# Performance work log

Measured on AMD Instinct MI355X. Metric: run time of the kernel, lower is better.

The kernel has to match this reference:

```python
import jax, jax.numpy as jnp
import numpy as np

B = 32        # graphs per batch
MAXN = 2048   # max nodes per graph (dense batch length)
HEADS = 8
DH = 64       # head dim (512/8)
M = 256       # FAVOR+ random features
D = 512
EPS = 1e-5    # batchnorm eps
KEPS = 1e-6   # performer stabilizer


def _batchnorm(x, g, b):
    # torch BatchNorm1d training-mode: biased batch statistics over node dim
    mu = jnp.mean(x, axis=0)
    var = jnp.mean((x - mu) ** 2, axis=0)
    return (x - mu) * jax.lax.rsqrt(var + EPS) * g + b


def setup_inputs() -> dict:
    key = jax.random.key(0)
    ks = jax.random.split(key, 10)
    sizes = 1024 + (np.arange(B) * 131) % 1025   # ragged graph sizes in [1024, 2048]
    N = int(sizes.sum())                          # 48544
    E = N * 8
    batch = jnp.asarray(np.repeat(np.arange(B), sizes), dtype=jnp.int32)
    edge_index = jax.random.randint(ks[0], (2, E), 0, N, dtype=jnp.int32)
    s = 1.0 / np.sqrt(D)
    return {
        'x': jax.random.normal(ks[1], (N, D), jnp.float32),
        'batch': batch,
        'edge_index': edge_index,
        'norm1_g': jnp.ones((D,), jnp.float32),
        'norm1_b': jnp.zeros((D,), jnp.float32),
        'norm2_g': jnp.ones((D,), jnp.float32),
        'norm2_b': jnp.zeros((D,), jnp.float32),
        'W_conv': jax.random.normal(ks[2], (D, D), jnp.float32) * s,
        'b_conv': jnp.zeros((D,), jnp.float32),
        'Wq': jax.random.normal(ks[3], (D, D), jnp.float32) * s,
        'Wk': jax.random.normal(ks[4], (D, D), jnp.float32) * s,
        'Wv': jax.random.normal(ks[5], (D, D), jnp.float32) * s,
        'Wo': jax.random.normal(ks[6], (D, D), jnp.float32) * s,
        'proj': jax.random.normal(ks[7], (M, DH), jnp.float32),
    }


def _forward(x, batch, edge_index, norm1_g, norm1_b, norm2_g, norm2_b,
             W_conv, b_conv, Wq, Wk, Wv, Wo, proj):
    N = x.shape[0]
    E = edge_index.shape[1]
    h = x

    # norm1 (+ dropout p=0 -> identity) then local GNN conv (mean-agg GCN + linear + relu)
    xn = _batchnorm(x, norm1_g, norm1_b)
    msg = xn[edge_index[0]]                                        # [E, D] gather
    agg = jax.ops.segment_sum(msg, edge_index[1], num_segments=N)  # [N, D] scatter-add
    deg = jax.ops.segment_sum(jnp.ones((E,), x.dtype), edge_index[1], num_segments=N)
    agg = agg / jnp.maximum(deg, 1.0)[:, None]
    conv_out = jax.nn.relu(agg @ W_conv + b_conv)

    # to_dense_batch(h, batch) -> h_dense [B, MAXN, D], mask [B, MAXN]
    counts = jax.ops.segment_sum(jnp.ones((N,), jnp.int32), batch, num_segments=B)
    offsets = jnp.concatenate([jnp.zeros((1,), jnp.int32), jnp.cumsum(counts)[:-1]])
    pos = jnp.arange(N, dtype=jnp.int32) - offsets[batch]
    h_dense = jnp.zeros((B, MAXN, D), x.dtype).at[batch, pos].set(h)
    mask = jnp.zeros((B, MAXN), bool).at[batch, pos].set(True)

    # Performer FAVOR+ non-causal self-attention
    def heads(t, W):
        return (t @ W).reshape(B, MAXN, HEADS, DH).transpose(0, 2, 1, 3)  # [B,H,MAXN,DH]
    q, k, v = heads(h_dense, Wq), heads(h_dense, Wk), heads(h_dense, Wv)

    scale = DH ** -0.25  # data normalizer applied to q and k each

    def phi(t, is_query):
        t = t * scale
        u = jnp.einsum('bhnd,md->bhnm', t, proj)           # [B,H,MAXN,M]
        diag = 0.5 * jnp.sum(t * t, axis=-1, keepdims=True)
        if is_query:
            m_ = jnp.max(u, axis=-1, keepdims=True)
        else:
            m_ = jnp.max(u, axis=(-2, -1), keepdims=True)
        return jnp.exp(u - diag - jax.lax.stop_gradient(m_)) / np.sqrt(M) + KEPS

    qf = phi(q, True)
    kf = phi(k, False) * mask[:, None, :, None]   # zero padded keys
    vm = v * mask[:, None, :, None]

    kv = jnp.einsum('bhnm,bhnd->bhmd', kf, vm)                    # [B,H,M,DH]
    z = 1.0 / (jnp.einsum('bhnm,bhm->bhn', qf, kf.sum(axis=2)) + KEPS)
    attn = jnp.einsum('bhnm,bhmd->bhnd', qf, kv) * z[..., None]   # [B,H,MAXN,DH]
    attn = attn.transpose(0, 2, 1, 3).reshape(B, MAXN, D) @ Wo

    h_attn = attn[batch, pos]                                      # gather back: [mask]

    return _batchnorm(conv_out + h_attn + h, norm2_g, norm2_b)


def reference(x, batch, edge_index, norm1_g, norm1_b, norm2_g, norm2_b,
              W_conv, b_conv, Wq, Wk, Wv, Wo, proj):
    return _forward(x, batch, edge_index, norm1_g, norm1_b, norm2_g, norm2_b,
                    W_conv, b_conv, Wq, Wk, Wv, Wo, proj)
```

## Files before the change

kernel.cpp:

```cpp
#include <hip/hip_runtime.h>
#include <stdint.h>

#define CDIV(a,b) (((a)+(b)-1)/(b))

typedef __attribute__((ext_vector_type(4))) float f32x4;
typedef __attribute__((ext_vector_type(8))) short s16x8;
typedef __attribute__((ext_vector_type(8))) unsigned short u16x8;
typedef __attribute__((ext_vector_type(4))) unsigned short u16x4;

__device__ __forceinline__ float bf2f(unsigned short u) {
  union { unsigned int i; float f; } c; c.i = ((unsigned int)u) << 16; return c.f;
}
__device__ __forceinline__ unsigned short f2bf(float f) {
  union { float f; unsigned int i; } c; c.f = f;
  unsigned int u = c.i;
  u += 0x7fffu + ((u >> 16) & 1u);
  return (unsigned short)(u >> 16);
}

#define KVROWS 80

template<int BM, int BN, int WM, int WN, int EPI, int GSWAP>
__global__ __launch_bounds__(256) void gemm_bt(
    const unsigned short* __restrict__ A, const unsigned short* __restrict__ B,
    void* __restrict__ Cout, const float* __restrict__ aux,
    int K, int lda, int ldb, int ldc, long zsC, int Mstore)
{
  constexpr int MT = BM / (WM * 16);
  constexpr int NT = BN / (WN * 16);
  constexpr int LDT = 40;
  __shared__ unsigned short As[BM * LDT];
  __shared__ unsigned short Bs[BN * LDT];
  const int tid = threadIdx.x, wid = tid >> 6, lane = tid & 63;
  const int l15 = lane & 15, hi = lane >> 4;
  const int wr = wid / WN, wc = wid % WN;
  const int bx = GSWAP ? blockIdx.y : blockIdx.x;
  const int by = GSWAP ? blockIdx.x : blockIdx.y;
  long m0 = (long)by * BM;
  const int n0 = bx * BN;
  f32x4 acc[MT][NT] = {};
  for (int k0 = 0; k0 < K; k0 += 32) {
    #pragma unroll
    for (int c = tid; c < BM * 4; c += 256) {
      int row = c >> 2, c8 = (c & 3) * 8;
      *(u16x8*)(&As[row * LDT + c8]) = *(const u16x8*)(A + (m0 + row) * lda + k0 + c8);
    }
    #pragma unroll
    for (int c = tid; c < BN * 4; c += 256) {
      int row = c >> 2, c8 = (c & 3) * 8;
      *(u16x8*)(&Bs[row * LDT + c8]) = *(const u16x8*)(B + (long)(n0 + row) * ldb + k0 + c8);
    }
    __syncthreads();
    s16x8 af[MT], bfv[NT];
    #pragma unroll
    for (int mt = 0; mt < MT; mt++)
      af[mt] = *(const s16x8*)(&As[(wr * MT * 16 + mt * 16 + l15) * LDT + hi * 8]);
    #pragma unroll
    for (int nt = 0; nt < NT; nt++)
      bfv[nt] = *(const s16x8*)(&Bs[(wc * NT * 16 + nt * 16 + l15) * LDT + hi * 8]);
    #pragma unroll
    for (int mt = 0; mt < MT; mt++)
      #pragma unroll
      for (int nt = 0; nt < NT; nt++)
        acc[mt][nt] = __builtin_amdgcn_mfma_f32_16x16x32_bf16(bfv[nt], af[mt], acc[mt][nt], 0, 0, 0);
    __syncthreads();
  }
  #pragma unroll
  for (int mt = 0; mt < MT; mt++) {
    long r = m0 + wr * (MT * 16) + mt * 16 + l15;
    if (r < Mstore) {
      #pragma unroll
      for (int nt = 0; nt < NT; nt++) {
        const int col0 = n0 + wc * (NT * 16) + nt * 16 + hi * 4;
        f32x4 v = acc[mt][nt];
        if constexpr (EPI == 7) {
          u16x4 o;
          #pragma unroll
          for (int i = 0; i < 4; i++) o[i] = f2bf(v[i]);
          *(u16x4*)((unsigned short*)Cout + (long)(col0 >> 6) * zsC + r * 64 + (col0 & 63)) = o;
        } else if constexpr (EPI == 8) {
          const f32x4 ax = *(const f32x4*)(aux + r * ldc + col0);
          f32x4 o;
          #pragma unroll
          for (int i = 0; i < 4; i++) o[i] = v[i] + ax[i];
          *(f32x4*)((float*)Cout + r * ldc + col0) = o;
        }
      }
    }
  }
}

__global__ __launch_bounds__(256) void gemm_conv_bn(
    const unsigned short* __restrict__ A, const unsigned short* __restrict__ B,
    float* __restrict__ out, const float* __restrict__ bias,
    float* __restrict__ s1, float* __restrict__ s2, int Mstore)
{
  constexpr int LDT = 40;
  __shared__ unsigned short As[128 * LDT];
  __shared__ unsigned short Bs[128 * LDT];
  const int tid = threadIdx.x, wid = tid >> 6, lane = tid & 63;
  const int l15 = lane & 15, hi = lane >> 4;
  const int wr = wid >> 1, wc = wid & 1;
  long m0 = (long)blockIdx.y * 128;
  const int n0 = blockIdx.x * 128;
  f32x4 acc[4][4] = {};
  for (int k0 = 0; k0 < 512; k0 += 32) {
    #pragma unroll
    for (int c = tid; c < 512; c += 256) {
      int row = c >> 2, c8 = (c & 3) * 8;
      *(u16x8*)(&As[row * LDT + c8]) = *(const u16x8*)(A + (m0 + row) * 512 + k0 + c8);
      *(u16x8*)(&Bs[row * LDT + c8]) = *(const u16x8*)(B + (long)(n0 + row) * 512 + k0 + c8);
    }
    __syncthreads();
    s16x8 af[4], bfv[4];
    #pragma unroll
    for (int mt = 0; mt < 4; mt++)
      af[mt] = *(const s16x8*)(&As[(wr * 64 + mt * 16 + l15) * LDT + hi * 8]);
    #pragma unroll
    for (int nt = 0; nt < 4; nt++)
      bfv[nt] = *(const s16x8*)(&Bs[(wc * 64 + nt * 16 + l15) * LDT + hi * 8]);
    #pragma unroll
    for (int mt = 0; mt < 4; mt++)
      #pragma unroll
      for (int nt = 0; nt < 4; nt++)
        acc[mt][nt] = __builtin_amdgcn_mfma_f32_16x16x32_bf16(bfv[nt], af[mt], acc[mt][nt], 0, 0, 0);
    __syncthreads();
  }
  float st[4][4] = {};
  float sq[4][4] = {};
  #pragma unroll
  for (int mt = 0; mt < 4; mt++) {
    long r = m0 + wr * 64 + mt * 16 + l15;
    bool valid = r < Mstore;
    #pragma unroll
    for (int nt = 0; nt < 4; nt++) {
      const int col0 = n0 + wc * 64 + nt * 16 + hi * 4;
      f32x4 o = {0.f, 0.f, 0.f, 0.f};
      if (valid) {
        float* cp = out + r * 512 + col0;
        f32x4 cur = *(f32x4*)cp;
        #pragma unroll
        for (int i = 0; i < 4; i++) {
          float cv = acc[mt][nt][i] + bias[col0 + i];
          cv = cv > 0.f ? cv : 0.f;
          o[i] = cur[i] + cv;
        }
        *(f32x4*)cp = o;
      }
      #pragma unroll
      for (int i = 0; i < 4; i++) { st[nt][i] += o[i]; sq[nt][i] += o[i] * o[i]; }
    }
  }
  #pragma unroll
  for (int nt = 0; nt < 4; nt++)
    #pragma unroll
    for (int i = 0; i < 4; i++) {
      float a = st[nt][i], b = sq[nt][i];
      a += __shfl_xor(a, 1); a += __shfl_xor(a, 2); a += __shfl_xor(a, 4); a += __shfl_xor(a, 8);
      b += __shfl_xor(b, 1); b += __shfl_xor(b, 2); b += __shfl_xor(b, 4); b += __shfl_xor(b, 8);
      if (l15 == 0) {
        const int col = n0 + wc * 64 + nt * 16 + hi * 4 + i;
        atomicAdd(&s1[col], a);
        atomicAdd(&s2[col], b);
      }
    }
}

__global__ __launch_bounds__(256, 4) void k_kmax(
    const unsigned short* __restrict__ kvqh, const unsigned short* __restrict__ projb,
    const unsigned int* __restrict__ offs, unsigned int* __restrict__ kmax, long Npad) {
  __shared__ float wmax[4];
  const int tid = threadIdx.x, wid = tid >> 6, lane = tid & 63;
  const int bh = blockIdx.x & 255, xb = blockIdx.x >> 8;
  const int b = bh >> 3, h = bh & 7;
  const unsigned int off = offs[b];
  const int nb = (int)(offs[b + 1] - off);
  const int m0 = xb * 64;
  if (m0 >= nb) return;
  const unsigned short* A = kvqh + ((long)(8 + h) * Npad + off + m0) * 64;
  f32x4 acc[4][4] = {};
  #pragma unroll
  for (int k0 = 0; k0 < 64; k0 += 32) {
    s16x8 af[4], bfv[4];
    #pragma unroll
    for (int mt = 0; mt < 4; mt++)
      af[mt] = *(const s16x8*)(A + (long)(mt * 16 + (lane & 15)) * 64 + k0 + ((lane >> 4) * 8));
    #pragma unroll
    for (int nt = 0; nt < 4; nt++)
      bfv[nt] = *(const s16x8*)(projb + (long)(wid * 64 + nt * 16 + (lane & 15)) * 64 + k0 + ((lane >> 4) * 8));
    #pragma unroll
    for (int mt = 0; mt < 4; mt++)
      #pragma unroll
      for (int nt = 0; nt < 4; nt++)
        acc[mt][nt] = __builtin_amdgcn_mfma_f32_16x16x32_bf16(af[mt], bfv[nt], acc[mt][nt], 0, 0, 0);
  }
  float bm = -3.0e38f;
  #pragma unroll
  for (int mt = 0; mt < 4; mt++)
    #pragma unroll
    for (int i = 0; i < 4; i++) {
      int row = mt * 16 + ((lane >> 4) << 2) + i;
      if (m0 + row < nb) {
        #pragma unroll
        for (int nt = 0; nt < 4; nt++) bm = fmaxf(bm, acc[mt][nt][i]);
      }
    }
  #pragma unroll
  for (int s = 1; s < 64; s <<= 1) bm = fmaxf(bm, __shfl_xor(bm, s));
  if (lane == 0) wmax[wid] = bm;
  __syncthreads();
  if (tid == 0) {
    float m = fmaxf(fmaxf(wmax[0], wmax[1]), fmaxf(wmax[2], wmax[3]));
    atomicMax(&kmax[b * 8 + h], __float_as_uint(fmaxf(m, 0.f)));
  }
}

__global__ __launch_bounds__(256) void k_kvm(
    const unsigned short* __restrict__ kvqh, const unsigned short* __restrict__ projb,
    const unsigned int* __restrict__ offs, const unsigned int* __restrict__ kmax,
    unsigned short* __restrict__ kvTb, long Npad) {
  constexpr int TLD = 72;
  __shared__ unsigned short vsT[2][64 * TLD];
  __shared__ unsigned short kfsT[64 * TLD];
  const int tid = threadIdx.x, wid = tid >> 6, lane = tid & 63;
  const int bh = blockIdx.x & 255, mblk = blockIdx.x >> 8;
  const int b = bh >> 3, h = bh & 7;
  const unsigned int off = offs[b];
  const int nb = (int)(offs[b + 1] - off);
  const float km = __uint_as_float(kmax[b * 8 + h]);
  const unsigned short* Kp = kvqh + ((long)(8 + h) * Npad + off) * 64;
  const unsigned short* Vp = kvqh + ((long)(16 + h) * Npad + off) * 64;
  const unsigned short* Pp = projb + (long)(mblk * 64 + wid * 16) * 64;
  const int l15 = lane & 15, hi = lane >> 4;
  const int mloc = wid * 16 + l15;

  #pragma unroll
  for (int c = tid; c < 512; c += 256) {
    int row = c >> 3, c8 = (c & 7) * 8;
    int rot = (c & 7) * 8;
    u16x8 v = *(const u16x8*)(Vp + (long)row * 64 + c8);
    #pragma unroll
    for (int j = 0; j < 8; j++) vsT[0][(c8 + j) * TLD + ((row + rot) & 63)] = v[j];
  }
  __syncthreads();

  f32x4 akv[4] = {};
  float ksum = 0.f;
  int buf = 0;
  for (int n0 = 0; n0 < nb; n0 += 64) {
    f32x4 acc[4] = {};
    float dsum[4] = {0.f, 0.f, 0.f, 0.f};
    #pragma unroll
    for (int k0 = 0; k0 < 64; k0 += 32) {
      s16x8 af[4];
      #pragma unroll
      for (int mt = 0; mt < 4; mt++)
        af[mt] = *(const s16x8*)(Kp + ((long)n0 + mt * 16 + l15) * 64 + k0 + hi * 8);
      s16x8 bfv = *(const s16x8*)(Pp + (long)l15 * 64 + k0 + hi * 8);
      #pragma unroll
      for (int mt = 0; mt < 4; mt++) {
        #pragma unroll
        for (int j = 0; j < 8; j++) {
          float a = bf2f((unsigned short)af[mt][j]);
          dsum[mt] += a * a;
        }
        acc[mt] = __builtin_amdgcn_mfma_f32_16x16x32_bf16(af[mt], bfv, acc[mt], 0, 0, 0);
      }
    }
    float rs[4];
    #pragma unroll
    for (int mt = 0; mt < 4; mt++) {
      float s = dsum[mt];
      s += __shfl_xor(s, 16); s += __shfl_xor(s, 32);
      rs[mt] = 0.0625f * s;
    }
    #pragma unroll
    for (int mt = 0; mt < 4; mt++) {
      int r0 = mt * 16 + hi * 4;
      float e[4];
      #pragma unroll
      for (int i = 0; i < 4; i++) {
        float dg = __shfl(rs[mt], hi * 4 + i);
        e[i] = (n0 + r0 + i < nb) ? (__expf(acc[mt][i] - dg - km) * 0.0625f + 1e-6f) : 0.f;
      }
      ksum += e[0] + e[1] + e[2] + e[3];
      unsigned int p0 = (unsigned int)f2bf(e[0]) | ((unsigned int)f2bf(e[1]) << 16);
      unsigned int p1 = (unsigned int)f2bf(e[2]) | ((unsigned int)f2bf(e[3]) << 16);
      *(unsigned int*)(&kfsT[mloc * TLD + r0]) = p0;
      *(unsigned int*)(&kfsT[mloc * TLD + r0 + 2]) = p1;
    }
    if (n0 + 64 < nb) {
      #pragma unroll
      for (int c = tid; c < 512; c += 256) {
        int row = c >> 3, c8 = (c & 7) * 8;
        int rot = (c & 7) * 8;
        u16x8 v = *(const u16x8*)(Vp + ((long)n0 + 64 + row) * 64 + c8);
        #pragma unroll
        for (int j = 0; j < 8; j++) vsT[buf ^ 1][(c8 + j) * TLD + ((row + rot) & 63)] = v[j];
      }
    }
    #pragma unroll
    for (int ks = 0; ks < 2; ks++) {
      s16x8 bB = *(const s16x8*)(&kfsT[mloc * TLD + ks * 32 + hi * 8]);
      #pragma unroll
      for (int mt2 = 0; mt2 < 4; mt2++) {
        int d = mt2 * 16 + l15;
        int rrot = ((ks * 32 + hi * 8) + ((d >> 3) & 7) * 8) & 63;
        s16x8 aA = *(const s16x8*)(&vsT[buf][d * TLD + rrot]);
        akv[mt2] = __builtin_amdgcn_mfma_f32_16x16x32_bf16(aA, bB, akv[mt2], 0, 0, 0);
      }
    }
    __syncthreads();
    buf ^= 1;
  }
  long base = ((long)b * 8 + h) * (KVROWS * 256);
  const int m = mblk * 64 + mloc;
  #pragma unroll
  for (int mt2 = 0; mt2 < 4; mt2++)
    #pragma unroll
    for (int i = 0; i < 4; i++) {
      int d = mt2 * 16 + hi * 4 + i;
      kvTb[base + (long)d * 256 + m] = f2bf(akv[mt2][i]);
    }
  ksum += __shfl_xor(ksum, 16); ksum += __shfl_xor(ksum, 32);
  if (hi == 0) kvTb[base + 64 * 256 + m] = f2bf(ksum);
}

__global__ __launch_bounds__(256, 4) void k_qflash(
    const unsigned short* __restrict__ qh_all, const unsigned short* __restrict__ projb,
    const unsigned short* __restrict__ kvTb, const unsigned int* __restrict__ offs,
    unsigned short* __restrict__ attn, long Npad) {
  constexpr int QLDT = 264;
  __shared__ unsigned short qfs[64 * QLDT];
  __shared__ float sdiag[64];
  __shared__ float smax[4][64];
  const int tid = threadIdx.x, wid = tid >> 6, lane = tid & 63;
  const int l15 = lane & 15, hi = lane >> 4;
  const int bh = blockIdx.x & 255, xb = blockIdx.x >> 8;
  const int b = bh >> 3, h = bh & 7;
  const unsigned int off = offs[b];
  const int nb = (int)(offs[b + 1] - off);
  const int m0 = xb * 64;
  if (m0 >= nb) return;
  const unsigned short* A = qh_all + ((long)h * Npad + off + m0) * 64;
  f32x4 acc[4][4] = {};
  float dsum[4] = {0.f, 0.f, 0.f, 0.f};
  #pragma unroll
  for (int k0 = 0; k0 < 64; k0 += 32) {
    s16x8 af[4], bfv[4];
    #pragma unroll
    for (int mt = 0; mt < 4; mt++)
      af[mt] = *(const s16x8*)(A + (long)(mt * 16 + l15) * 64 + k0 + hi * 8);
    #pragma unroll
    for (int nt = 0; nt < 4; nt++)
      bfv[nt] = *(const s16x8*)(projb + (long)(wid * 64 + nt * 16 + l15) * 64 + k0 + hi * 8);
    if (wid == 0) {
      #pragma unroll
      for (int mt = 0; mt < 4; mt++)
        #pragma unroll
        for (int j = 0; j < 8; j++) {
          float a = bf2f((unsigned short)af[mt][j]);
          dsum[mt] += a * a;
        }
    }
    #pragma unroll
    for (int mt = 0; mt < 4; mt++)
      #pragma unroll
      for (int nt = 0; nt < 4; nt++)
        acc[mt][nt] = __builtin_amdgcn_mfma_f32_16x16x32_bf16(af[mt], bfv[nt], acc[mt][nt], 0, 0, 0);
  }
  if (wid == 0) {
    #pragma unroll
    for (int mt = 0; mt < 4; mt++) {
      float s = dsum[mt];
      s += __shfl_xor(s, 16); s += __shfl_xor(s, 32);
      if (lane < 16) sdiag[mt * 16 + lane] = 0.0625f * s;
    }
  }
  #pragma unroll
  for (int mt = 0; mt < 4; mt++)
    #pragma unroll
    for (int i = 0; i < 4; i++) {
      float rm = fmaxf(fmaxf(acc[mt][0][i], acc[mt][1][i]), fmaxf(acc[mt][2][i], acc[mt][3][i]));
      rm = fmaxf(rm, __shfl_xor(rm, 1)); rm = fmaxf(rm, __shfl_xor(rm, 2));
      rm = fmaxf(rm, __shfl_xor(rm, 4)); rm = fmaxf(rm, __shfl_xor(rm, 8));
      if (l15 == 0) smax[wid][mt * 16 + hi * 4 + i] = rm;
    }
  __syncthreads();
  #pragma unroll
  for (int mt = 0; mt < 4; mt++)
    #pragma unroll
    for (int i = 0; i < 4; i++) {
      int row = mt * 16 + hi * 4 + i;
      float rm = fmaxf(fmaxf(smax[0][row], smax[1][row]), fmaxf(smax[2][row], smax[3][row]));
      float sub = sdiag[row] + rm;
      #pragma unroll
      for (int nt = 0; nt < 4; nt++) {
        int col = wid * 64 + nt * 16 + l15;
        qfs[row * QLDT + col] = f2bf(__expf(acc[mt][nt][i] - sub) * 0.0625f + 1e-6f);
      }
    }
  __syncthreads();
  const unsigned short* kvb = kvTb + ((long)b * 8 + h) * (KVROWS * 256);
  f32x4 acc2[4] = {};
  f32x4 acc3 = {};
  #pragma unroll
  for (int ks = 0; ks < 8; ks++) {
    s16x8 aq = *(const s16x8*)(&qfs[(wid * 16 + l15) * QLDT + ks * 32 + hi * 8]);
    #pragma unroll
    for (int t = 0; t < 4; t++) {
      s16x8 bk = *(const s16x8*)(kvb + (long)(t * 16 + l15) * 256 + ks * 32 + hi * 8);
      acc2[t] = __builtin_amdgcn_mfma_f32_16x16x32_bf16(aq, bk, acc2[t], 0, 0, 0);
    }
    s16x8 bz = *(const s16x8*)(kvb + (long)(64 + l15) * 256 + ks * 32 + hi * 8);
    acc3 = __builtin_amdgcn_mfma_f32_16x16x32_bf16(aq, bz, acc3, 0, 0, 0);
  }
  float zr[4];
  #pragma unroll
  for (int i = 0; i < 4; i++) {
    float zden = __shfl(acc3[i], hi * 16);
    zr[i] = 1.f / (zden + 1e-6f);
  }
  #pragma unroll
  for (int t = 0; t < 4; t++)
    #pragma unroll
    for (int i = 0; i < 4; i++) {
      int row = wid * 16 + hi * 4 + i;
      if (m0 + row < nb)
        attn[(long)(off + m0 + row) * 512 + h * 64 + t * 16 + l15] = f2bf(acc2[t][i] * zr[i]);
    }
}


__global__ void k_fill(float* __restrict__ out, long n, float v) {
  long i = (long)blockIdx.x * 256 + threadIdx.x;
  if (i < n) out[i] = v;
}

__global__ void k_convx_stats(const float* __restrict__ x, unsigned short* __restrict__ xb,
                              float* __restrict__ s1, float* __restrict__ s2, int N, int rpb) {
  int t = threadIdx.x;
  int r0 = blockIdx.x * rpb;
  int r1 = min(N, r0 + rpb);
  float a1 = 0, a2 = 0, b1 = 0, b2 = 0;
  for (int r = r0; r < r1; r++) {
    const float* xr = x + (long)r * 512 + 2 * t;
    float va = xr[0], vb = xr[1];
    a1 += va; a2 += va * va; b1 += vb; b2 += vb * vb;
    *(unsigned int*)(xb + (long)r * 512 + 2 * t) =
        (unsigned int)f2bf(va) | ((unsigned int)f2bf(vb) << 16);
  }
  atomicAdd(&s1[2 * t], a1); atomicAdd(&s2[2 * t], a2);
  atomicAdd(&s1[2 * t + 1], b1); atomicAdd(&s2[2 * t + 1], b2);
}

__global__ void k_transall(const float* __restrict__ w0, const float* __restrict__ w1,
                           const float* __restrict__ w2, const float* __restrict__ w3,
                           const float* __restrict__ w4, unsigned short* __restrict__ out) {
  long idx = (long)blockIdx.x * 256 + threadIdx.x;
  if (idx >= (5L << 18)) return;
  int which = (int)(idx >> 18);
  int r = (int)(idx & 262143);
  int n = r >> 9, k = r & 511;
  const float* w = which == 0 ? w0 : which == 1 ? w1 : which == 2 ? w2 : which == 3 ? w3 : w4;
  out[idx] = f2bf(w[k * 512 + n]);
}

__global__ void k_scale_copy_bf(const float* __restrict__ in, unsigned short* __restrict__ out,
                                int n, float scl) {
  int i = blockIdx.x * 256 + threadIdx.x;
  if (i < n) out[i] = f2bf(in[i] * scl);
}

__global__ void k_bn_final(const float* __restrict__ s1, const float* __restrict__ s2,
                           const float* __restrict__ g, const float* __restrict__ b,
                           float* __restrict__ a, float* __restrict__ c, float invN) {
  int t = threadIdx.x;
  float mu = s1[t] * invN;
  float var = s2[t] * invN - mu * mu;
  float inv = rsqrtf(var + 1e-5f);
  float av = g[t] * inv;
  a[t] = av;
  c[t] = b[t] - mu * av;
}

__global__ void k_deg(const int* __restrict__ ed, unsigned int* __restrict__ deg, long E) {
  long i = (long)blockIdx.x * 256 + threadIdx.x;
  if (i < E) atomicAdd(&deg[ed[i]], 1u);
}

__global__ void k_offs(const int* __restrict__ batch, unsigned int* __restrict__ offs, int N) {
  int i = blockIdx.x * 256 + threadIdx.x;
  if (i >= N) return;
  int b = batch[i];
  if (i == 0) { for (int bb = 0; bb <= b; bb++) offs[bb] = 0; }
  else {
    int pb = batch[i - 1];
    if (pb != b) for (int bb = pb + 1; bb <= b; bb++) offs[bb] = i;
  }
  if (i == N - 1) { for (int bb = b + 1; bb <= 32; bb++) offs[bb] = N; }
}

__global__ __launch_bounds__(1024) void k_scan_nodes(const unsigned int* __restrict__ deg,
                                                     unsigned int* __restrict__ rowstart, int N) {
  __shared__ unsigned int wsum[16];
  __shared__ unsigned int carry_s;
  int t = threadIdx.x, lane = t & 63, wid = t >> 6;
  if (t == 0) carry_s = 0;
  __syncthreads();
  for (int base = 0; base < N; base += 1024) {
    int i = base + t;
    unsigned int v = (i < N) ? deg[i] : 0;
    unsigned int sc = v;
    #pragma unroll
    for (int s = 1; s < 64; s <<= 1) {
      unsigned int u = __shfl_up(sc, s);
      if (lane >= s) sc += u;
    }
    if (lane == 63) wsum[wid] = sc;
    __syncthreads();
    unsigned int woff = 0, tot = 0;
    #pragma unroll
    for (int w = 0; w < 16; w++) { unsigned int s = wsum[w]; if (w < wid) woff += s; tot += s; }
    unsigned int carry = carry_s;
    if (i < N) rowstart[i] = carry + woff + sc - v;
    __syncthreads();
    if (t == 0) carry_s = carry + tot;
    __syncthreads();
  }
  if (threadIdx.x == 0) rowstart[N] = carry_s;
}

__global__ void k_csr_fill(const int* __restrict__ es, const int* __restrict__ ed,
                           const unsigned int* __restrict__ rowstart,
                           unsigned int* __restrict__ cursor, int* __restrict__ csr, long E) {
  long e = (long)blockIdx.x * 256 + threadIdx.x;
  if (e >= E) return;
  int d = ed[e];
  unsigned int slot = atomicAdd(&cursor[d], 1u);
  csr[rowstart[d] + slot] = es[e];
}

__global__ __launch_bounds__(128) void k_gather(const int* __restrict__ csr,
                                                const unsigned int* __restrict__ rowstart,
                                                const unsigned short* __restrict__ xb,
                                                const float* __restrict__ a1, const float* __restrict__ c1,
                                                unsigned short* __restrict__ conv_in, int N) {
  long n = blockIdx.x;
  int c = threadIdx.x * 4;
  u16x4 o; o[0] = 0; o[1] = 0; o[2] = 0; o[3] = 0;
  if (n < N) {
    unsigned int r0 = rowstart[n], r1 = rowstart[n + 1];
    if (r1 > r0) {
      f32x4 acc0 = {}, acc1 = {};
      unsigned int j = r0;
      for (; j + 2 <= r1; j += 2) {
        u16x4 v0 = *(const u16x4*)(xb + (long)csr[j] * 512 + c);
        u16x4 v1 = *(const u16x4*)(xb + (long)csr[j + 1] * 512 + c);
        #pragma unroll
        for (int i = 0; i < 4; i++) { acc0[i] += bf2f(v0[i]); acc1[i] += bf2f(v1[i]); }
      }
      if (j < r1) {
        u16x4 v0 = *(const u16x4*)(xb + (long)csr[j] * 512 + c);
        #pragma unroll
        for (int i = 0; i < 4; i++) acc0[i] += bf2f(v0[i]);
      }
      f32x4 acc = acc0 + acc1;
      float inv = 1.f / (float)(r1 - r0);
      o[0] = f2bf(acc[0] * inv * a1[c + 0] + c1[c + 0]);
      o[1] = f2bf(acc[1] * inv * a1[c + 1] + c1[c + 1]);
      o[2] = f2bf(acc[2] * inv * a1[c + 2] + c1[c + 2]);
      o[3] = f2bf(acc[3] * inv * a1[c + 3] + c1[c + 3]);
    }
  }
  *(u16x4*)(conv_in + n * 512 + c) = o;
}

__global__ void k_bn_apply(float* __restrict__ y, const float* __restrict__ a,
                           const float* __restrict__ c, long total) {
  long i4 = ((long)blockIdx.x * 256 + threadIdx.x) * 4;
  if (i4 >= total) return;
  int col = (int)(i4 & 511);
  f32x4 v = *(const f32x4*)(y + i4);
  #pragma unroll
  for (int j = 0; j < 4; j++) v[j] = v[j] * a[col + j] + c[col + j];
  *(f32x4*)(y + i4) = v;
}


extern "C" void kernel_launch(void* const* d_in, const int* in_sizes, int n_in,
                              void* d_out, int out_size, void* d_ws, size_t ws_size,
                              hipStream_t stream) {
  (void)n_in; (void)out_size;
  const float* x = (const float*)d_in[0];
  const int* batch = (const int*)d_in[1];
  const int* eidx = (const int*)d_in[2];
  const float* n1g = (const float*)d_in[3];
  const float* n1b = (const float*)d_in[4];
  const float* n2g = (const float*)d_in[5];
  const float* n2b = (const float*)d_in[6];
  const float* wconv = (const float*)d_in[7];
  const float* bconv = (const float*)d_in[8];
  const float* wq = (const float*)d_in[9];
  const float* wk = (const float*)d_in[10];
  const float* wv = (const float*)d_in[11];
  const float* wo = (const float*)d_in[12];
  const float* proj = (const float*)d_in[13];

  const int N = in_sizes[1];
  const long E = in_sizes[2] / 2;
  const long Npad = CDIV(N, 128) * 128 + 256;
  const int Mb = (int)((CDIV(N, 128) * 128 + 128) / 128);
  const int MbC = CDIV(N, 128);
  const int* es = eidx;
  const int* ed = eidx + E;
  float* out = (float*)d_out;

  char* p = (char*)d_ws;
  auto alloc = [&](size_t bytes) -> char* {
    char* r = p;
    p += (bytes + 255) & ~(size_t)255;
    return r;
  };
  unsigned short* kvqh = (unsigned short*)alloc((size_t)24 * Npad * 64 * 2);
  unsigned short* xbf  = (unsigned short*)alloc((size_t)Npad * 512 * 2);
  unsigned short* conv_in = (unsigned short*)alloc((size_t)Npad * 512 * 2);
  unsigned short* kvT_b = (unsigned short*)alloc((size_t)32 * 8 * KVROWS * 256 * 2);
  unsigned short* wts   = (unsigned short*)alloc((size_t)5 * 512 * 512 * 2);
  unsigned short* proj_s = (unsigned short*)alloc((size_t)256 * 64 * 2);
  float* bn1_acc = (float*)alloc(1024 * 4);
  float* bn1_ac  = (float*)alloc(1024 * 4);
  float* bn2_acc = (float*)alloc(1024 * 4);
  float* bn2_ac  = (float*)alloc(1024 * 4);
  unsigned int* deg      = (unsigned int*)alloc((size_t)N * 4);
  unsigned int* offs     = (unsigned int*)alloc(33 * 4);
  unsigned int* kmax     = (unsigned int*)alloc(32 * 8 * 4);
  unsigned int* rowstart = (unsigned int*)alloc((size_t)(N + 1) * 4);
  unsigned int* cursor   = (unsigned int*)alloc((size_t)N * 4);
  int* csr               = (int*)alloc((size_t)E * 4);
  size_t required = (size_t)(p - (char*)d_ws);
  if (required > ws_size) {
    k_fill<<<(int)CDIV((long)N * 512, 256), 256, 0, stream>>>(
        out, (long)N * 512, 1.0e6f + (float)(ws_size >> 20));
    return;
  }
  unsigned short* wqkv_t  = wts;
  unsigned short* wconv_t = wts + 3 * 512 * 512;
  unsigned short* wo_t    = wts + 4 * 512 * 512;
  unsigned short* attn2   = kvqh + (size_t)8 * Npad * 64;

  hipMemsetAsync(deg, 0, (size_t)N * 4, stream);
  hipMemsetAsync(cursor, 0, (size_t)N * 4, stream);
  hipMemsetAsync(kmax, 0, 32 * 8 * 4, stream);
  hipMemsetAsync(bn1_acc, 0, 1024 * 4, stream);
  hipMemsetAsync(bn2_acc, 0, 1024 * 4, stream);
  hipMemsetAsync(xbf + (size_t)N * 512, 0, (size_t)(Npad - N) * 512 * 2, stream);

  int rpb = CDIV(N, 1024);
  k_convx_stats<<<1024, 256, 0, stream>>>(x, xbf, bn1_acc, bn1_acc + 512, N, rpb);
  k_transall<<<(int)CDIV(5L << 18, 256), 256, 0, stream>>>(wq, wk, wv, wconv, wo, wts);
  k_scale_copy_bf<<<CDIV(256 * 64, 256), 256, 0, stream>>>(proj, proj_s, 256 * 64, 0.35355339059327373f);
  k_bn_final<<<1, 512, 0, stream>>>(bn1_acc, bn1_acc + 512, n1g, n1b, bn1_ac, bn1_ac + 512, 1.f / N);
  k_deg<<<(int)CDIV(E, 256), 256, 0, stream>>>(ed, deg, E);
  k_offs<<<CDIV(N, 256), 256, 0, stream>>>(batch, offs, N);
  k_scan_nodes<<<1, 1024, 0, stream>>>(deg, rowstart, N);
  k_csr_fill<<<(int)CDIV(E, 256), 256, 0, stream>>>(es, ed, rowstart, cursor, csr, E);

  gemm_bt<128, 128, 2, 2, 7, 1><<<dim3(Mb, 12), 256, 0, stream>>>(
      xbf, wqkv_t, kvqh, nullptr, 512, 512, 512, 0, (long)Npad * 64, (int)Npad);

  k_kmax<<<32 * 256, 256, 0, stream>>>(kvqh, proj_s, offs, kmax, Npad);
  k_kvm<<<4 * 256, 256, 0, stream>>>(kvqh, proj_s, offs, kmax, kvT_b, Npad);

  k_gather<<<MbC * 128, 128, 0, stream>>>(csr, rowstart, xbf, bn1_ac, bn1_ac + 512, conv_in, N);

  k_qflash<<<32 * 256, 256, 0, stream>>>(
      kvqh, proj_s, kvT_b, offs, attn2, Npad);

  gemm_bt<128, 128, 2, 2, 8, 0><<<dim3(4, MbC), 256, 0, stream>>>(
      attn2, wo_t, out, x, 512, 512, 512, 512, 0, N);

  gemm_conv_bn<<<dim3(4, MbC), 256, 0, stream>>>(
      conv_in, wconv_t, out, bconv, bn2_acc, bn2_acc + 512, N);

  k_bn_final<<<1, 512, 0, stream>>>(bn2_acc, bn2_acc + 512, n2g, n2b, bn2_ac, bn2_ac + 512, 1.f / N);
  k_bn_apply<<<(int)CDIV((long)N * 512 / 4, 256), 256, 0, stream>>>(out, bn2_ac, bn2_ac + 512, (long)N * 512);
}
```

Before: 1.050 ms.

## Swap MFMA operands in qflash, prefetch kv fragments, add setprio, reorder GEMM grids

In the query feature kernel, the MFMA operands are swapped so each lane owns a full row. That lets every wave compute the diagonal term, the row max and the normaliser locally, and write vectorized 4-element bf16 stores instead of scattered 2-byte ones. The kv fragments are now register double-buffered across the k-steps, and s_setprio brackets are added around MFMA bursts in several kernels. The output and conv GEMM grids are transposed so row tiles vary fastest, which changes L2 reuse of the weight tiles. In exchange, register pressure rises from the prefetch buffers, and all waves now redundantly compute the diagonal.

```diff
diff --git a/kernel.cpp b/kernel.cpp
--- a/kernel.cpp
+++ b/kernel.cpp
@@ -101,8 +101,8 @@
   const int tid = threadIdx.x, wid = tid >> 6, lane = tid & 63;
   const int l15 = lane & 15, hi = lane >> 4;
   const int wr = wid >> 1, wc = wid & 1;
-  long m0 = (long)blockIdx.y * 128;
-  const int n0 = blockIdx.x * 128;
+  long m0 = (long)blockIdx.x * 128;
+  const int n0 = blockIdx.y * 128;
   f32x4 acc[4][4] = {};
   for (int k0 = 0; k0 < 512; k0 += 32) {
     #pragma unroll
@@ -188,11 +188,13 @@
     #pragma unroll
     for (int nt = 0; nt < 4; nt++)
       bfv[nt] = *(const s16x8*)(projb + (long)(wid * 64 + nt * 16 + (lane & 15)) * 64 + k0 + ((lane >> 4) * 8));
+    __builtin_amdgcn_s_setprio(1);
     #pragma unroll
     for (int mt = 0; mt < 4; mt++)
       #pragma unroll
       for (int nt = 0; nt < 4; nt++)
         acc[mt][nt] = __builtin_amdgcn_mfma_f32_16x16x32_bf16(af[mt], bfv[nt], acc[mt][nt], 0, 0, 0);
+    __builtin_amdgcn_s_setprio(0);
   }
   float bm = -3.0e38f;
   #pragma unroll
@@ -257,6 +259,7 @@
       for (int mt = 0; mt < 4; mt++)
         af[mt] = *(const s16x8*)(Kp + ((long)n0 + mt * 16 + l15) * 64 + k0 + hi * 8);
       s16x8 bfv = *(const s16x8*)(Pp + (long)l15 * 64 + k0 + hi * 8);
+      __builtin_amdgcn_s_setprio(1);
       #pragma unroll
       for (int mt = 0; mt < 4; mt++) {
         #pragma unroll
@@ -266,6 +269,7 @@
         }
         acc[mt] = __builtin_amdgcn_mfma_f32_16x16x32_bf16(af[mt], bfv, acc[mt], 0, 0, 0);
       }
+      __builtin_amdgcn_s_setprio(0);
     }
     float rs[4];
     #pragma unroll
@@ -299,6 +303,7 @@
         for (int j = 0; j < 8; j++) vsT[buf ^ 1][(c8 + j) * TLD + ((row + rot) & 63)] = v[j];
       }
     }
+    __builtin_amdgcn_s_setprio(1);
     #pragma unroll
     for (int ks = 0; ks < 2; ks++) {
       s16x8 bB = *(const s16x8*)(&kfsT[mloc * TLD + ks * 32 + hi * 8]);
@@ -310,6 +315,7 @@
         akv[mt2] = __builtin_amdgcn_mfma_f32_16x16x32_bf16(aA, bB, akv[mt2], 0, 0, 0);
       }
     }
+    __builtin_amdgcn_s_setprio(0);
     __syncthreads();
     buf ^= 1;
   }
@@ -332,7 +338,6 @@
     unsigned short* __restrict__ attn, long Npad) {
   constexpr int QLDT = 264;
   __shared__ unsigned short qfs[64 * QLDT];
-  __shared__ float sdiag[64];
   __shared__ float smax[4][64];
   const int tid = threadIdx.x, wid = tid >> 6, lane = tid & 63;
   const int l15 = lane & 15, hi = lane >> 4;
@@ -343,6 +348,7 @@
   const int m0 = xb * 64;
   if (m0 >= nb) return;
   const unsigned short* A = qh_all + ((long)h * Npad + off + m0) * 64;
+
   f32x4 acc[4][4] = {};
   float dsum[4] = {0.f, 0.f, 0.f, 0.f};
   #pragma unroll
@@ -354,81 +360,96 @@
     #pragma unroll
     for (int nt = 0; nt < 4; nt++)
       bfv[nt] = *(const s16x8*)(projb + (long)(wid * 64 + nt * 16 + l15) * 64 + k0 + hi * 8);
-    if (wid == 0) {
-      #pragma unroll
-      for (int mt = 0; mt < 4; mt++)
-        #pragma unroll
-        for (int j = 0; j < 8; j++) {
-          float a = bf2f((unsigned short)af[mt][j]);
-          dsum[mt] += a * a;
-        }
-    }
     #pragma unroll
     for (int mt = 0; mt < 4; mt++)
       #pragma unroll
+      for (int j = 0; j < 8; j++) {
+        float a = bf2f((unsigned short)af[mt][j]);
+        dsum[mt] += a * a;
+      }
+    __builtin_amdgcn_s_setprio(1);
+    #pragma unroll
+    for (int mt = 0; mt < 4; mt++)
+      #pragma unroll
       for (int nt = 0; nt < 4; nt++)
-        acc[mt][nt] = __builtin_amdgcn_mfma_f32_16x16x32_bf16(af[mt], bfv[nt], acc[mt][nt], 0, 0, 0);
-  }
-  if (wid == 0) {
-    #pragma unroll
-    for (int mt = 0; mt < 4; mt++) {
-      float s = dsum[mt];
-      s += __shfl_xor(s, 16); s += __shfl_xor(s, 32);
-      if (lane < 16) sdiag[mt * 16 + lane] = 0.0625f * s;
-    }
-  }
-  #pragma unroll
-  for (int mt = 0; mt < 4; mt++)
-    #pragma unroll
-    for (int i = 0; i < 4; i++) {
-      float rm = fmaxf(fmaxf(acc[mt][0][i], acc[mt][1][i]), fmaxf(acc[mt][2][i], acc[mt][3][i]));
-      rm = fmaxf(rm, __shfl_xor(rm, 1)); rm = fmaxf(rm, __shfl_xor(rm, 2));
-      rm = fmaxf(rm, __shfl_xor(rm, 4)); rm = fmaxf(rm, __shfl_xor(rm, 8));
-      if (l15 == 0) smax[wid][mt * 16 + hi * 4 + i] = rm;
-    }
+        acc[mt][nt] = __builtin_amdgcn_mfma_f32_16x16x32_bf16(bfv[nt], af[mt], acc[mt][nt], 0, 0, 0);
+    __builtin_amdgcn_s_setprio(0);
+  }
+  float diag[4];
+  #pragma unroll
+  for (int mt = 0; mt < 4; mt++) {
+    float s = dsum[mt];
+    s += __shfl_xor(s, 16); s += __shfl_xor(s, 32);
+    diag[mt] = 0.0625f * s;
+  }
+  float rmax[4];
+  #pragma unroll
+  for (int mt = 0; mt < 4; mt++) {
+    float m = acc[mt][0][0];
+    #pragma unroll
+    for (int nt = 0; nt < 4; nt++)
+      #pragma unroll
+      for (int i = 0; i < 4; i++) m = fmaxf(m, acc[mt][nt][i]);
+    m = fmaxf(m, __shfl_xor(m, 16)); m = fmaxf(m, __shfl_xor(m, 32));
+    rmax[mt] = m;
+    if (hi == 0) smax[wid][mt * 16 + l15] = m;
+  }
   __syncthreads();
   #pragma unroll
-  for (int mt = 0; mt < 4; mt++)
-    #pragma unroll
-    for (int i = 0; i < 4; i++) {
-      int row = mt * 16 + hi * 4 + i;
-      float rm = fmaxf(fmaxf(smax[0][row], smax[1][row]), fmaxf(smax[2][row], smax[3][row]));
-      float sub = sdiag[row] + rm;
-      #pragma unroll
-      for (int nt = 0; nt < 4; nt++) {
-        int col = wid * 64 + nt * 16 + l15;
-        qfs[row * QLDT + col] = f2bf(__expf(acc[mt][nt][i] - sub) * 0.0625f + 1e-6f);
-      }
-    }
+  for (int mt = 0; mt < 4; mt++) {
+    int row = mt * 16 + l15;
+    float rm = fmaxf(fmaxf(smax[0][row], smax[1][row]), fmaxf(smax[2][row], smax[3][row]));
+    float sub = diag[mt] + rm;
+    #pragma unroll
+    for (int nt = 0; nt < 4; nt++) {
+      u16x4 o;
+      #pragma unroll
+      for (int i = 0; i < 4; i++)
+        o[i] = f2bf(__expf(acc[mt][nt][i] - sub) * 0.0625f + 1e-6f);
+      *(u16x4*)(&qfs[row * QLDT + wid * 64 + nt * 16 + hi * 4]) = o;
+    }
+  }
   __syncthreads();
   const unsigned short* kvb = kvTb + ((long)b * 8 + h) * (KVROWS * 256);
   f32x4 acc2[4] = {};
   f32x4 acc3 = {};
+  s16x8 bkc[5];
+  #pragma unroll
+  for (int t = 0; t < 5; t++)
+    bkc[t] = *(const s16x8*)(kvb + (long)(t * 16 + l15) * 256 + hi * 8);
   #pragma unroll
   for (int ks = 0; ks < 8; ks++) {
+    s16x8 bkn[5];
+    if (ks < 7) {
+      #pragma unroll
+      for (int t = 0; t < 5; t++)
+        bkn[t] = *(const s16x8*)(kvb + (long)(t * 16 + l15) * 256 + (ks + 1) * 32 + hi * 8);
+    }
     s16x8 aq = *(const s16x8*)(&qfs[(wid * 16 + l15) * QLDT + ks * 32 + hi * 8]);
+    __builtin_amdgcn_s_setprio(1);
+    #pragma unroll
+    for (int t = 0; t < 4; t++)
+      acc2[t] = __builtin_amdgcn_mfma_f32_16x16x32_bf16(bkc[t], aq, acc2[t], 0, 0, 0);
+    acc3 = __builtin_amdgcn_mfma_f32_16x16x32_bf16(bkc[4], aq, acc3, 0, 0, 0);
+    __builtin_amdgcn_s_setprio(0);
+    if (ks < 7) {
+      #pragma unroll
+      for (int t = 0; t < 5; t++) bkc[t] = bkn[t];
+    }
+  }
+  float zden = __shfl(acc3[0], l15);
+  float zr = 1.f / (zden + 1e-6f);
+  int row = wid * 16 + l15;
+  if (m0 + row < nb) {
+    unsigned short* po = attn + (long)(off + m0 + row) * 512 + h * 64;
     #pragma unroll
     for (int t = 0; t < 4; t++) {
-      s16x8 bk = *(const s16x8*)(kvb + (long)(t * 16 + l15) * 256 + ks * 32 + hi * 8);
-      acc2[t] = __builtin_amdgcn_mfma_f32_16x16x32_bf16(aq, bk, acc2[t], 0, 0, 0);
-    }
-    s16x8 bz = *(const s16x8*)(kvb + (long)(64 + l15) * 256 + ks * 32 + hi * 8);
-    acc3 = __builtin_amdgcn_mfma_f32_16x16x32_bf16(aq, bz, acc3, 0, 0, 0);
-  }
-  float zr[4];
-  #pragma unroll
-  for (int i = 0; i < 4; i++) {
-    float zden = __shfl(acc3[i], hi * 16);
-    zr[i] = 1.f / (zden + 1e-6f);
-  }
-  #pragma unroll
-  for (int t = 0; t < 4; t++)
-    #pragma unroll
-    for (int i = 0; i < 4; i++) {
-      int row = wid * 16 + hi * 4 + i;
-      if (m0 + row < nb)
-        attn[(long)(off + m0 + row) * 512 + h * 64 + t * 16 + l15] = f2bf(acc2[t][i] * zr[i]);
-    }
+      u16x4 o;
+      #pragma unroll
+      for (int i = 0; i < 4; i++) o[i] = f2bf(acc2[t][i] * zr);
+      *(u16x4*)(po + t * 16 + hi * 4) = o;
+    }
+  }
 }
 
 
@@ -677,10 +698,10 @@
   k_qflash<<<32 * 256, 256, 0, stream>>>(
       kvqh, proj_s, kvT_b, offs, attn2, Npad);
 
-  gemm_bt<128, 128, 2, 2, 8, 0><<<dim3(4, MbC), 256, 0, stream>>>(
+  gemm_bt<128, 128, 2, 2, 8, 1><<<dim3(MbC, 4), 256, 0, stream>>>(
       attn2, wo_t, out, x, 512, 512, 512, 512, 0, N);
 
-  gemm_conv_bn<<<dim3(4, MbC), 256, 0, stream>>>(
+  gemm_conv_bn<<<dim3(MbC, 4), 256, 0, stream>>>(
       conv_in, wconv_t, out, bconv, bn2_acc, bn2_acc + 512, N);
 
   k_bn_final<<<1, 512, 0, stream>>>(bn2_acc, bn2_acc + 512, n2g, n2b, bn2_ac, bn2_ac + 512, 1.f / N);
```

After: 1.130 ms. 1.08x slower.
